# Kernel tuning notes

Hardware: AMD Instinct MI355X
Metric: run time of the kernel (lower is better)

The kernel has to match this reference:

```python
import jax, jax.numpy as jnp
import numpy as np

NUM_TOKENS = 2048
NUM_HEADS = 32
NUM_KV_HEADS = 8
HEAD_DIM = 128
ATTN_SCALE = 0.08838834764831845  # 1/sqrt(head_dim)


def setup_inputs() -> dict:
    key = jax.random.key(0)
    kq, kk, kv = jax.random.split(key, 3)
    q = jax.random.normal(kq, (NUM_TOKENS, NUM_HEADS, HEAD_DIM), dtype=jnp.float32)
    k = jax.random.normal(kk, (NUM_TOKENS, NUM_KV_HEADS, HEAD_DIM), dtype=jnp.float32)
    v = jax.random.normal(kv, (NUM_TOKENS, NUM_KV_HEADS, HEAD_DIM), dtype=jnp.float32)
    return {"q": q, "k": k, "v": v}


def reference(q, k, v):
    # Prefill path: all tokens attend causally; GQA expands kv heads.
    n_rep = NUM_HEADS // NUM_KV_HEADS
    k = jnp.repeat(k, n_rep, axis=1)  # (T, H, D)
    v = jnp.repeat(v, n_rep, axis=1)  # (T, H, D)
    # scores: (H, Tq, Tk)
    scores = jnp.einsum("thd,shd->hts", q, k) * ATTN_SCALE
    T = q.shape[0]
    causal = jnp.tril(jnp.ones((T, T), dtype=bool))  # (Tq, Tk)
    scores = jnp.where(causal[None, :, :], scores, -jnp.inf)
    weights = jax.nn.softmax(scores, axis=-1)
    out = jnp.einsum("hts,shd->thd", weights, v)  # (T, H, D)
    return out
```

## Files before the change

kernel.cpp:

```cpp
#include <hip/hip_runtime.h>

#define NT 2048
#define NH 32
#define NKV 8
#define HD 128
#define BM 128
#define BN 64
#define NQT (NT / BM)
#define SCALE_LOG2E 0.12754984003389239f
#define NEG_BIG -1.0e30f

typedef unsigned int   uint4v  __attribute__((ext_vector_type(4)));
typedef unsigned int   uint2v  __attribute__((ext_vector_type(2)));
typedef float          f32x4   __attribute__((ext_vector_type(4)));
typedef __bf16         bf16x8  __attribute__((ext_vector_type(8)));
typedef unsigned short u16;

#define PK 136
#define PV 72
#define PP 72
#define PO 136

__device__ __forceinline__ float bf2f(unsigned u) {
  return __builtin_bit_cast(float, u << 16);
}
__device__ __forceinline__ unsigned f2bf(float f) {
  unsigned u = __builtin_bit_cast(unsigned, f);
  u += 0x7fffu + ((u >> 16) & 1u);
  return u >> 16;
}

__global__ __launch_bounds__(256, 2)
void prep_kernel(const float* __restrict__ kg, const float* __restrict__ vg,
                 u16* __restrict__ wsk, u16* __restrict__ wsv) {
  __shared__ __align__(16) u16 lds_v[HD * PV];
  const int tid  = threadIdx.x;
  const int lane = tid & 63;
  const int w    = tid >> 6;
  const int hk   = blockIdx.x >> 5;
  const int jt   = blockIdx.x & 31;
  const int kv0  = jt * 64;

#pragma unroll
  for (int rr = 0; rr < 4; ++rr) {
    const int flat = rr * 256 + tid;
    const int row = flat >> 4, ch = flat & 15;
    const float* kp = &kg[((kv0 + row) * NKV + hk) * HD + ch * 8];
    const f32x4 a = *(const f32x4*)kp;
    const f32x4 b = *(const f32x4*)(kp + 4);
    uint4v pk;
    pk[0] = f2bf(a[0]) | (f2bf(a[1]) << 16);
    pk[1] = f2bf(a[2]) | (f2bf(a[3]) << 16);
    pk[2] = f2bf(b[0]) | (f2bf(b[1]) << 16);
    pk[3] = f2bf(b[2]) | (f2bf(b[3]) << 16);
    *(uint4v*)&wsk[(hk * NT + kv0 + row) * HD + ch * 8] = pk;
  }
#pragma unroll
  for (int rr = 0; rr < 4; ++rr) {
    const int d0 = (rr * 4 + w) * 8;
    const float* vp = &vg[((kv0 + lane) * NKV + hk) * HD + d0];
    const f32x4 a = *(const f32x4*)vp;
    const f32x4 b = *(const f32x4*)(vp + 4);
#pragma unroll
    for (int e = 0; e < 4; ++e) {
      lds_v[(d0 + e) * PV + lane]     = (u16)f2bf(a[e]);
      lds_v[(d0 + 4 + e) * PV + lane] = (u16)f2bf(b[e]);
    }
  }
  __syncthreads();
#pragma unroll
  for (int rr = 0; rr < 4; ++rr) {
    const int flat = rr * 256 + tid;
    const int row = flat >> 3, ch = flat & 7;
    *(uint4v*)&wsv[(hk * HD + row) * NT + kv0 + ch * 8] =
        *(uint4v*)&lds_v[row * PV + ch * 8];
  }
}

template <bool PRE>
__global__ __launch_bounds__(256, 2)
void fa_kernel(const float* __restrict__ qg, const float* __restrict__ kg,
               const float* __restrict__ vg, float* __restrict__ og,
               const u16* __restrict__ wsk, const u16* __restrict__ wsv) {
  __shared__ __align__(16) u16 lds_k[64 * PK];
  __shared__ __align__(16) u16 lds_v[HD * PV];
  __shared__ __align__(16) u16 lds_p[4 * 32 * PP];

  const int tid  = threadIdx.x;
  const int lane = tid & 63;
  const int w    = tid >> 6;
  const int quad = lane >> 4;
  const int l16  = lane & 15;

  const int h  = blockIdx.x;
  const int hk = h >> 2;
  const int y  = (int)blockIdx.y;
  const int qt = (y < NQT / 2) ? (NQT - 1 - y) : (y - NQT / 2);
  const int q0  = qt * BM;
  const int q0w = q0 + w * 32;

  uint4v qf[2][4];
#pragma unroll
  for (int qn = 0; qn < 2; ++qn)
#pragma unroll
    for (int c = 0; c < 4; ++c) {
      const int row = q0w + qn * 16 + l16;
      const float* qp = &qg[(row * NH + h) * HD + c * 32 + quad * 8];
      const f32x4 a = *(const f32x4*)qp;
      const f32x4 b = *(const f32x4*)(qp + 4);
      uint4v r;
      r[0] = f2bf(a[0] * SCALE_LOG2E) | (f2bf(a[1] * SCALE_LOG2E) << 16);
      r[1] = f2bf(a[2] * SCALE_LOG2E) | (f2bf(a[3] * SCALE_LOG2E) << 16);
      r[2] = f2bf(b[0] * SCALE_LOG2E) | (f2bf(b[1] * SCALE_LOG2E) << 16);
      r[3] = f2bf(b[2] * SCALE_LOG2E) | (f2bf(b[3] * SCALE_LOG2E) << 16);
      qf[qn][c] = r;
    }

  f32x4 o[8][2];
#pragma unroll
  for (int nt = 0; nt < 8; ++nt)
#pragma unroll
    for (int qn = 0; qn < 2; ++qn)
#pragma unroll
      for (int r = 0; r < 4; ++r) o[nt][qn][r] = 0.f;

  float l_run[2] = {0.f, 0.f};

  u16* pw = &lds_p[w * 32 * PP];

  const int njt = 2 * qt + 2;
  for (int jt = 0; jt < njt; ++jt) {
    const int kv0 = jt * BN;
    __syncthreads();

    if (PRE) {
#pragma unroll
      for (int rr = 0; rr < 4; ++rr) {
        const int flat = rr * 256 + tid;
        const int row = flat >> 4, ch = flat & 15;
        *(uint4v*)&lds_k[row * PK + ch * 8] =
            *(const uint4v*)&wsk[(hk * NT + kv0 + row) * HD + ch * 8];
      }
#pragma unroll
      for (int rr = 0; rr < 4; ++rr) {
        const int flat = rr * 256 + tid;
        const int row = flat >> 3, ch = flat & 7;
        *(uint4v*)&lds_v[row * PV + ch * 8] =
            *(const uint4v*)&wsv[(hk * HD + row) * NT + kv0 + ch * 8];
      }
    } else {
#pragma unroll
      for (int rr = 0; rr < 4; ++rr) {
        const int flat = rr * 256 + tid;
        const int row = flat >> 4, ch = flat & 15;
        const float* kp = &kg[((kv0 + row) * NKV + hk) * HD + ch * 8];
        const f32x4 a = *(const f32x4*)kp;
        const f32x4 b = *(const f32x4*)(kp + 4);
        uint4v pk;
        pk[0] = f2bf(a[0]) | (f2bf(a[1]) << 16);
        pk[1] = f2bf(a[2]) | (f2bf(a[3]) << 16);
        pk[2] = f2bf(b[0]) | (f2bf(b[1]) << 16);
        pk[3] = f2bf(b[2]) | (f2bf(b[3]) << 16);
        *(uint4v*)&lds_k[row * PK + ch * 8] = pk;
      }
#pragma unroll
      for (int rr = 0; rr < 4; ++rr) {
        const int d0 = (rr * 4 + w) * 8;
        const float* vp = &vg[((kv0 + lane) * NKV + hk) * HD + d0];
        const f32x4 a = *(const f32x4*)vp;
        const f32x4 b = *(const f32x4*)(vp + 4);
#pragma unroll
        for (int e = 0; e < 4; ++e) {
          lds_v[(d0 + e) * PV + lane]     = (u16)f2bf(a[e]);
          lds_v[(d0 + 4 + e) * PV + lane] = (u16)f2bf(b[e]);
        }
      }
    }
    __syncthreads();

    if (kv0 > q0w + 31) continue;

    f32x4 s[4][2];
#pragma unroll
    for (int mt = 0; mt < 4; ++mt)
#pragma unroll
      for (int qn = 0; qn < 2; ++qn)
#pragma unroll
        for (int r = 0; r < 4; ++r) s[mt][qn][r] = 0.f;

#pragma unroll
    for (int c = 0; c < 4; ++c) {
#pragma unroll
      for (int mt = 0; mt < 4; ++mt) {
        const uint4v kf = *(uint4v*)&lds_k[(mt * 16 + l16) * PK + c * 32 + quad * 8];
#pragma unroll
        for (int qn = 0; qn < 2; ++qn)
          s[mt][qn] = __builtin_amdgcn_mfma_f32_16x16x32_bf16(
              __builtin_bit_cast(bf16x8, kf),
              __builtin_bit_cast(bf16x8, qf[qn][c]), s[mt][qn], 0, 0, 0);
      }
    }

    if (kv0 + BN - 1 > q0w) {
#pragma unroll
      for (int mt = 0; mt < 4; ++mt)
#pragma unroll
        for (int qn = 0; qn < 2; ++qn)
#pragma unroll
          for (int r = 0; r < 4; ++r) {
            const int kvgl = kv0 + mt * 16 + quad * 4 + r;
            const int qgl  = q0w + qn * 16 + l16;
            if (kvgl > qgl) s[mt][qn][r] = NEG_BIG;
          }
    }

#pragma unroll
    for (int qn = 0; qn < 2; ++qn) {
      float ts = 0.f;
#pragma unroll
      for (int mt = 0; mt < 4; ++mt)
#pragma unroll
        for (int r = 0; r < 4; ++r) {
          const float p = exp2f(s[mt][qn][r]);
          s[mt][qn][r] = p;
          ts += p;
        }
      ts += __shfl_xor(ts, 16);
      ts += __shfl_xor(ts, 32);
      l_run[qn] += ts;

#pragma unroll
      for (int mt = 0; mt < 4; ++mt) {
        uint2v pk2;
        pk2[0] = f2bf(s[mt][qn][0]) | (f2bf(s[mt][qn][1]) << 16);
        pk2[1] = f2bf(s[mt][qn][2]) | (f2bf(s[mt][qn][3]) << 16);
        *(uint2v*)&pw[(qn * 16 + l16) * PP + mt * 16 + quad * 4] = pk2;
      }
    }

    __asm__ __volatile__("s_waitcnt lgkmcnt(0)" ::: "memory");

#pragma unroll
    for (int c2 = 0; c2 < 2; ++c2) {
      uint4v pf[2];
#pragma unroll
      for (int qn = 0; qn < 2; ++qn)
        pf[qn] = *(uint4v*)&pw[(qn * 16 + l16) * PP + c2 * 32 + quad * 8];
#pragma unroll
      for (int nt = 0; nt < 8; ++nt) {
        const uint4v vf = *(uint4v*)&lds_v[(nt * 16 + l16) * PV + c2 * 32 + quad * 8];
#pragma unroll
        for (int qn = 0; qn < 2; ++qn)
          o[nt][qn] = __builtin_amdgcn_mfma_f32_16x16x32_bf16(
              __builtin_bit_cast(bf16x8, vf),
              __builtin_bit_cast(bf16x8, pf[qn]), o[nt][qn], 0, 0, 0);
      }
    }
  }

  __syncthreads();

  u16* ob = (w < 2) ? &lds_k[w * 32 * PO] : &lds_v[(w - 2) * 32 * PO];

#pragma unroll
  for (int qn = 0; qn < 2; ++qn) {
    const float inv = 1.0f / l_run[qn];
#pragma unroll
    for (int nt = 0; nt < 8; ++nt) {
      uint2v ok2;
      ok2[0] = f2bf(o[nt][qn][0] * inv) | (f2bf(o[nt][qn][1] * inv) << 16);
      ok2[1] = f2bf(o[nt][qn][2] * inv) | (f2bf(o[nt][qn][3] * inv) << 16);
      *(uint2v*)&ob[(qn * 16 + l16) * PO + nt * 16 + quad * 4] = ok2;
    }
  }
  __asm__ __volatile__("s_waitcnt lgkmcnt(0)" ::: "memory");
#pragma unroll
  for (int rr = 0; rr < 8; ++rr) {
    const int idx = rr * 64 + lane;
    const int row = idx >> 4, ch = idx & 15;
    const uint4v ov = *(uint4v*)&ob[row * PO + ch * 8];
    f32x4 lo, hi;
    lo[0] = bf2f(ov[0] & 0xffffu); lo[1] = bf2f(ov[0] >> 16);
    lo[2] = bf2f(ov[1] & 0xffffu); lo[3] = bf2f(ov[1] >> 16);
    hi[0] = bf2f(ov[2] & 0xffffu); hi[1] = bf2f(ov[2] >> 16);
    hi[2] = bf2f(ov[3] & 0xffffu); hi[3] = bf2f(ov[3] >> 16);
    float* op = &og[((q0 + w * 32 + row) * NH + h) * HD + ch * 8];
    *(f32x4*)op       = lo;
    *(f32x4*)(op + 4) = hi;
  }
}

extern "C" void kernel_launch(void* const* d_in, const int* in_sizes, int n_in,
                              void* d_out, int out_size, void* d_ws, size_t ws_size,
                              hipStream_t stream) {
  (void)in_sizes; (void)n_in; (void)out_size;
  const float* q = (const float*)d_in[0];
  const float* k = (const float*)d_in[1];
  const float* v = (const float*)d_in[2];
  float* out = (float*)d_out;

  const size_t kv_bytes = (size_t)NKV * NT * HD * 2;
  dim3 grid(NH, NQT);
  if (ws_size >= 2 * kv_bytes) {
    u16* wsk = (u16*)d_ws;
    u16* wsv = wsk + (size_t)NKV * NT * HD;
    prep_kernel<<<dim3(NKV * 32), dim3(256), 0, stream>>>(k, v, wsk, wsv);
    fa_kernel<true><<<grid, dim3(256), 0, stream>>>(q, k, v, out, wsk, wsv);
  } else {
    fa_kernel<false><<<grid, dim3(256), 0, stream>>>(q, k, v, out, nullptr, nullptr);
  }
}
```

Baseline: 169.1 us.

## Double-buffer K/V tiles, pass P via shuffles, and cheapen bf16 packing

The attention kernel now double-buffers K and V tiles in LDS with register prefetch, so the global loads for the next tile overlap the MFMA work on the current one and the loop needs one barrier per tile instead of two. The P matrix is rearranged across lanes with shuffles instead of a round trip through LDS. The row-sum reduction is deferred to the end, exp2 uses the hardware builtin, and bf16 conversion uses round-half-up with a perm-based pack in place of round-to-nearest-even. The prep kernel is rewritten with smaller tiles and twice as many blocks. In exchange the kernel holds more LDS and registers, which may reduce occupancy, and rounding differs slightly from the old code.

New measurement: 149.8 us. -11.4%, faster.

```diff
diff --git a/kernel.cpp b/kernel.cpp
--- a/kernel.cpp
+++ b/kernel.cpp
@@ -18,62 +18,56 @@
 
 #define PK 136
 #define PV 72
-#define PP 72
 #define PO 136
 
 __device__ __forceinline__ float bf2f(unsigned u) {
   return __builtin_bit_cast(float, u << 16);
 }
 __device__ __forceinline__ unsigned f2bf(float f) {
-  unsigned u = __builtin_bit_cast(unsigned, f);
-  u += 0x7fffu + ((u >> 16) & 1u);
-  return u >> 16;
+  return (__builtin_bit_cast(unsigned, f) + 0x8000u) >> 16;
+}
+__device__ __forceinline__ unsigned pack_rn(float lo, float hi) {
+  const unsigned ul = __builtin_bit_cast(unsigned, lo) + 0x8000u;
+  const unsigned uh = __builtin_bit_cast(unsigned, hi) + 0x8000u;
+  return __builtin_amdgcn_perm(ul, uh, 0x03020706u);
 }
 
 __global__ __launch_bounds__(256, 2)
 void prep_kernel(const float* __restrict__ kg, const float* __restrict__ vg,
                  u16* __restrict__ wsk, u16* __restrict__ wsv) {
-  __shared__ __align__(16) u16 lds_v[HD * PV];
-  const int tid  = threadIdx.x;
-  const int lane = tid & 63;
-  const int w    = tid >> 6;
-  const int hk   = blockIdx.x >> 5;
-  const int jt   = blockIdx.x & 31;
-  const int kv0  = jt * 64;
-
-#pragma unroll
-  for (int rr = 0; rr < 4; ++rr) {
-    const int flat = rr * 256 + tid;
-    const int row = flat >> 4, ch = flat & 15;
-    const float* kp = &kg[((kv0 + row) * NKV + hk) * HD + ch * 8];
-    const f32x4 a = *(const f32x4*)kp;
-    const f32x4 b = *(const f32x4*)(kp + 4);
-    uint4v pk;
-    pk[0] = f2bf(a[0]) | (f2bf(a[1]) << 16);
-    pk[1] = f2bf(a[2]) | (f2bf(a[3]) << 16);
-    pk[2] = f2bf(b[0]) | (f2bf(b[1]) << 16);
-    pk[3] = f2bf(b[2]) | (f2bf(b[3]) << 16);
-    *(uint4v*)&wsk[(hk * NT + kv0 + row) * HD + ch * 8] = pk;
-  }
-#pragma unroll
-  for (int rr = 0; rr < 4; ++rr) {
-    const int d0 = (rr * 4 + w) * 8;
-    const float* vp = &vg[((kv0 + lane) * NKV + hk) * HD + d0];
-    const f32x4 a = *(const f32x4*)vp;
-    const f32x4 b = *(const f32x4*)(vp + 4);
-#pragma unroll
-    for (int e = 0; e < 4; ++e) {
-      lds_v[(d0 + e) * PV + lane]     = (u16)f2bf(a[e]);
-      lds_v[(d0 + 4 + e) * PV + lane] = (u16)f2bf(b[e]);
-    }
+  __shared__ __align__(16) float lds_f[32 * 132];
+  const int tid = threadIdx.x;
+  const int hk  = (int)blockIdx.x >> 6;
+  const int kv0 = ((int)blockIdx.x & 63) * 32;
+
+#pragma unroll
+  for (int r = 0; r < 4; ++r) {
+    const int flat = r * 256 + tid;
+    const int row = flat >> 5, q8 = flat & 31;
+    const f32x4 a = *(const f32x4*)&kg[((kv0 + row) * NKV + hk) * HD + q8 * 4];
+    uint2v pk;
+    pk[0] = pack_rn(a[0], a[1]);
+    pk[1] = pack_rn(a[2], a[3]);
+    *(uint2v*)&wsk[(hk * NT + kv0 + row) * HD + q8 * 4] = pk;
+  }
+#pragma unroll
+  for (int r = 0; r < 4; ++r) {
+    const int flat = r * 256 + tid;
+    const int row = flat >> 5, q8 = flat & 31;
+    *(f32x4*)&lds_f[row * 132 + q8 * 4] =
+        *(const f32x4*)&vg[((kv0 + row) * NKV + hk) * HD + q8 * 4];
   }
   __syncthreads();
-#pragma unroll
-  for (int rr = 0; rr < 4; ++rr) {
-    const int flat = rr * 256 + tid;
-    const int row = flat >> 3, ch = flat & 7;
-    *(uint4v*)&wsv[(hk * HD + row) * NT + kv0 + ch * 8] =
-        *(uint4v*)&lds_v[row * PV + ch * 8];
+  const int d = tid >> 1, half = tid & 1;
+#pragma unroll
+  for (int jj = 0; jj < 2; ++jj) {
+    const int j = half * 2 + jj;
+    uint4v outw;
+#pragma unroll
+    for (int e = 0; e < 4; ++e)
+      outw[e] = pack_rn(lds_f[(j * 8 + 2 * e) * 132 + d],
+                        lds_f[(j * 8 + 2 * e + 1) * 132 + d]);
+    *(uint4v*)&wsv[(hk * HD + d) * NT + kv0 + j * 8] = outw;
   }
 }
 
@@ -82,9 +76,8 @@
 void fa_kernel(const float* __restrict__ qg, const float* __restrict__ kg,
                const float* __restrict__ vg, float* __restrict__ og,
                const u16* __restrict__ wsk, const u16* __restrict__ wsv) {
-  __shared__ __align__(16) u16 lds_k[64 * PK];
-  __shared__ __align__(16) u16 lds_v[HD * PV];
-  __shared__ __align__(16) u16 lds_p[4 * 32 * PP];
+  __shared__ __align__(16) u16 lds_k[2][64 * PK];
+  __shared__ __align__(16) u16 lds_v[2][HD * PV];
 
   const int tid  = threadIdx.x;
   const int lane = tid & 63;
@@ -108,12 +101,12 @@
       const float* qp = &qg[(row * NH + h) * HD + c * 32 + quad * 8];
       const f32x4 a = *(const f32x4*)qp;
       const f32x4 b = *(const f32x4*)(qp + 4);
-      uint4v r;
-      r[0] = f2bf(a[0] * SCALE_LOG2E) | (f2bf(a[1] * SCALE_LOG2E) << 16);
-      r[1] = f2bf(a[2] * SCALE_LOG2E) | (f2bf(a[3] * SCALE_LOG2E) << 16);
-      r[2] = f2bf(b[0] * SCALE_LOG2E) | (f2bf(b[1] * SCALE_LOG2E) << 16);
-      r[3] = f2bf(b[2] * SCALE_LOG2E) | (f2bf(b[3] * SCALE_LOG2E) << 16);
-      qf[qn][c] = r;
+      uint4v rg;
+      rg[0] = pack_rn(a[0] * SCALE_LOG2E, a[1] * SCALE_LOG2E);
+      rg[1] = pack_rn(a[2] * SCALE_LOG2E, a[3] * SCALE_LOG2E);
+      rg[2] = pack_rn(b[0] * SCALE_LOG2E, b[1] * SCALE_LOG2E);
+      rg[3] = pack_rn(b[2] * SCALE_LOG2E, b[3] * SCALE_LOG2E);
+      qf[qn][c] = rg;
     }
 
   f32x4 o[8][2];
@@ -126,150 +119,189 @@
 
   float l_run[2] = {0.f, 0.f};
 
-  u16* pw = &lds_p[w * 32 * PP];
-
   const int njt = 2 * qt + 2;
+
+  uint4v kreg[4], vreg[4];
+  f32x4  kregf[4][2], vregf[4][2];
+
+  auto stage_load = [&](int jt) {
+    const int kvb = jt * BN;
+    if (PRE) {
+#pragma unroll
+      for (int r = 0; r < 4; ++r) {
+        const int flat = r * 256 + tid;
+        kreg[r] = *(const uint4v*)&wsk[(hk * NT + kvb + (flat >> 4)) * HD + (flat & 15) * 8];
+      }
+#pragma unroll
+      for (int r = 0; r < 4; ++r) {
+        const int flat = r * 256 + tid;
+        vreg[r] = *(const uint4v*)&wsv[(hk * HD + (flat >> 3)) * NT + kvb + (flat & 7) * 8];
+      }
+    } else {
+#pragma unroll
+      for (int r = 0; r < 4; ++r) {
+        const int flat = r * 256 + tid;
+        const float* kp = &kg[((kvb + (flat >> 4)) * NKV + hk) * HD + (flat & 15) * 8];
+        kregf[r][0] = *(const f32x4*)kp;
+        kregf[r][1] = *(const f32x4*)(kp + 4);
+      }
+#pragma unroll
+      for (int r = 0; r < 4; ++r) {
+        const int d0 = (r * 4 + w) * 8;
+        const float* vp = &vg[((kvb + lane) * NKV + hk) * HD + d0];
+        vregf[r][0] = *(const f32x4*)vp;
+        vregf[r][1] = *(const f32x4*)(vp + 4);
+      }
+    }
+  };
+  auto stage_write = [&](int b) {
+    if (PRE) {
+#pragma unroll
+      for (int r = 0; r < 4; ++r) {
+        const int flat = r * 256 + tid;
+        *(uint4v*)&lds_k[b][(flat >> 4) * PK + (flat & 15) * 8] = kreg[r];
+      }
+#pragma unroll
+      for (int r = 0; r < 4; ++r) {
+        const int flat = r * 256 + tid;
+        *(uint4v*)&lds_v[b][(flat >> 3) * PV + (flat & 7) * 8] = vreg[r];
+      }
+    } else {
+#pragma unroll
+      for (int r = 0; r < 4; ++r) {
+        const int flat = r * 256 + tid;
+        uint4v pk;
+        pk[0] = pack_rn(kregf[r][0][0], kregf[r][0][1]);
+        pk[1] = pack_rn(kregf[r][0][2], kregf[r][0][3]);
+        pk[2] = pack_rn(kregf[r][1][0], kregf[r][1][1]);
+        pk[3] = pack_rn(kregf[r][1][2], kregf[r][1][3]);
+        *(uint4v*)&lds_k[b][(flat >> 4) * PK + (flat & 15) * 8] = pk;
+      }
+#pragma unroll
+      for (int r = 0; r < 4; ++r) {
+        const int d0 = (r * 4 + w) * 8;
+#pragma unroll
+        for (int e = 0; e < 4; ++e) {
+          lds_v[b][(d0 + e) * PV + lane]     = (u16)f2bf(vregf[r][0][e]);
+          lds_v[b][(d0 + 4 + e) * PV + lane] = (u16)f2bf(vregf[r][1][e]);
+        }
+      }
+    }
+  };
+
+  const int sl0 = (quad & 1) * 32 + l16;
+  const int sl1 = sl0 + 16;
+  const bool qlo = (quad < 2);
+
+  stage_load(0);
+  stage_write(0);
+  __syncthreads();
+
   for (int jt = 0; jt < njt; ++jt) {
     const int kv0 = jt * BN;
-    __syncthreads();
-
-    if (PRE) {
-#pragma unroll
-      for (int rr = 0; rr < 4; ++rr) {
-        const int flat = rr * 256 + tid;
-        const int row = flat >> 4, ch = flat & 15;
-        *(uint4v*)&lds_k[row * PK + ch * 8] =
-            *(const uint4v*)&wsk[(hk * NT + kv0 + row) * HD + ch * 8];
-      }
-#pragma unroll
-      for (int rr = 0; rr < 4; ++rr) {
-        const int flat = rr * 256 + tid;
-        const int row = flat >> 3, ch = flat & 7;
-        *(uint4v*)&lds_v[row * PV + ch * 8] =
-            *(const uint4v*)&wsv[(hk * HD + row) * NT + kv0 + ch * 8];
-      }
-    } else {
-#pragma unroll
-      for (int rr = 0; rr < 4; ++rr) {
-        const int flat = rr * 256 + tid;
-        const int row = flat >> 4, ch = flat & 15;
-        const float* kp = &kg[((kv0 + row) * NKV + hk) * HD + ch * 8];
-        const f32x4 a = *(const f32x4*)kp;
-        const f32x4 b = *(const f32x4*)(kp + 4);
-        uint4v pk;
-        pk[0] = f2bf(a[0]) | (f2bf(a[1]) << 16);
-        pk[1] = f2bf(a[2]) | (f2bf(a[3]) << 16);
-        pk[2] = f2bf(b[0]) | (f2bf(b[1]) << 16);
-        pk[3] = f2bf(b[2]) | (f2bf(b[3]) << 16);
-        *(uint4v*)&lds_k[row * PK + ch * 8] = pk;
-      }
-#pragma unroll
-      for (int rr = 0; rr < 4; ++rr) {
-        const int d0 = (rr * 4 + w) * 8;
-        const float* vp = &vg[((kv0 + lane) * NKV + hk) * HD + d0];
-        const f32x4 a = *(const f32x4*)vp;
-        const f32x4 b = *(const f32x4*)(vp + 4);
-#pragma unroll
-        for (int e = 0; e < 4; ++e) {
-          lds_v[(d0 + e) * PV + lane]     = (u16)f2bf(a[e]);
-          lds_v[(d0 + 4 + e) * PV + lane] = (u16)f2bf(b[e]);
-        }
-      }
-    }
-    __syncthreads();
-
-    if (kv0 > q0w + 31) continue;
-
-    f32x4 s[4][2];
-#pragma unroll
-    for (int mt = 0; mt < 4; ++mt)
-#pragma unroll
-      for (int qn = 0; qn < 2; ++qn)
-#pragma unroll
-        for (int r = 0; r < 4; ++r) s[mt][qn][r] = 0.f;
-
-#pragma unroll
-    for (int c = 0; c < 4; ++c) {
-#pragma unroll
-      for (int mt = 0; mt < 4; ++mt) {
-        const uint4v kf = *(uint4v*)&lds_k[(mt * 16 + l16) * PK + c * 32 + quad * 8];
+    const int b   = jt & 1;
+    const bool havenext = (jt + 1 < njt);
+    if (havenext) stage_load(jt + 1);
+
+    if (kv0 <= q0w + 31) {
+      f32x4 s[4][2];
+#pragma unroll
+      for (int mt = 0; mt < 4; ++mt)
 #pragma unroll
         for (int qn = 0; qn < 2; ++qn)
-          s[mt][qn] = __builtin_amdgcn_mfma_f32_16x16x32_bf16(
-              __builtin_bit_cast(bf16x8, kf),
-              __builtin_bit_cast(bf16x8, qf[qn][c]), s[mt][qn], 0, 0, 0);
-      }
-    }
-
-    if (kv0 + BN - 1 > q0w) {
-#pragma unroll
-      for (int mt = 0; mt < 4; ++mt)
-#pragma unroll
-        for (int qn = 0; qn < 2; ++qn)
+#pragma unroll
+          for (int r = 0; r < 4; ++r) s[mt][qn][r] = 0.f;
+
+#pragma unroll
+      for (int c = 0; c < 4; ++c) {
+#pragma unroll
+        for (int mt = 0; mt < 4; ++mt) {
+          const uint4v kf = *(uint4v*)&lds_k[b][(mt * 16 + l16) * PK + c * 32 + quad * 8];
+#pragma unroll
+          for (int qn = 0; qn < 2; ++qn)
+            s[mt][qn] = __builtin_amdgcn_mfma_f32_16x16x32_bf16(
+                __builtin_bit_cast(bf16x8, kf),
+                __builtin_bit_cast(bf16x8, qf[qn][c]), s[mt][qn], 0, 0, 0);
+        }
+      }
+
+      if (kv0 + BN - 1 > q0w) {
+#pragma unroll
+        for (int mt = 0; mt < 4; ++mt)
+#pragma unroll
+          for (int qn = 0; qn < 2; ++qn)
+#pragma unroll
+            for (int r = 0; r < 4; ++r) {
+              const int kvgl = kv0 + mt * 16 + quad * 4 + r;
+              const int qgl  = q0w + qn * 16 + l16;
+              if (kvgl > qgl) s[mt][qn][r] = NEG_BIG;
+            }
+      }
+
+      unsigned pk[4][2][2];
+#pragma unroll
+      for (int qn = 0; qn < 2; ++qn) {
+        float ts = 0.f;
+#pragma unroll
+        for (int mt = 0; mt < 4; ++mt) {
 #pragma unroll
           for (int r = 0; r < 4; ++r) {
-            const int kvgl = kv0 + mt * 16 + quad * 4 + r;
-            const int qgl  = q0w + qn * 16 + l16;
-            if (kvgl > qgl) s[mt][qn][r] = NEG_BIG;
+            const float p = __builtin_amdgcn_exp2f(s[mt][qn][r]);
+            s[mt][qn][r] = p;
+            ts += p;
           }
-    }
-
-#pragma unroll
-    for (int qn = 0; qn < 2; ++qn) {
-      float ts = 0.f;
-#pragma unroll
-      for (int mt = 0; mt < 4; ++mt)
-#pragma unroll
-        for (int r = 0; r < 4; ++r) {
-          const float p = exp2f(s[mt][qn][r]);
-          s[mt][qn][r] = p;
-          ts += p;
-        }
-      ts += __shfl_xor(ts, 16);
-      ts += __shfl_xor(ts, 32);
-      l_run[qn] += ts;
-
-#pragma unroll
-      for (int mt = 0; mt < 4; ++mt) {
-        uint2v pk2;
-        pk2[0] = f2bf(s[mt][qn][0]) | (f2bf(s[mt][qn][1]) << 16);
-        pk2[1] = f2bf(s[mt][qn][2]) | (f2bf(s[mt][qn][3]) << 16);
-        *(uint2v*)&pw[(qn * 16 + l16) * PP + mt * 16 + quad * 4] = pk2;
-      }
-    }
-
-    __asm__ __volatile__("s_waitcnt lgkmcnt(0)" ::: "memory");
-
-#pragma unroll
-    for (int c2 = 0; c2 < 2; ++c2) {
-      uint4v pf[2];
-#pragma unroll
-      for (int qn = 0; qn < 2; ++qn)
-        pf[qn] = *(uint4v*)&pw[(qn * 16 + l16) * PP + c2 * 32 + quad * 8];
-#pragma unroll
-      for (int nt = 0; nt < 8; ++nt) {
-        const uint4v vf = *(uint4v*)&lds_v[(nt * 16 + l16) * PV + c2 * 32 + quad * 8];
-#pragma unroll
-        for (int qn = 0; qn < 2; ++qn)
-          o[nt][qn] = __builtin_amdgcn_mfma_f32_16x16x32_bf16(
-              __builtin_bit_cast(bf16x8, vf),
-              __builtin_bit_cast(bf16x8, pf[qn]), o[nt][qn], 0, 0, 0);
-      }
+          pk[mt][qn][0] = pack_rn(s[mt][qn][0], s[mt][qn][1]);
+          pk[mt][qn][1] = pack_rn(s[mt][qn][2], s[mt][qn][3]);
+        }
+        l_run[qn] += ts;
+      }
+
+#pragma unroll
+      for (int c2 = 0; c2 < 2; ++c2) {
+        uint4v pf[2];
+#pragma unroll
+        for (int p = 0; p < 4; ++p) {
+          const int sl = (p >> 1) ? sl1 : sl0;
+#pragma unroll
+          for (int qn = 0; qn < 2; ++qn) {
+            const int vA = __shfl((int)pk[2 * c2][qn][p & 1], sl);
+            const int vB = __shfl((int)pk[2 * c2 + 1][qn][p & 1], sl);
+            pf[qn][p] = (unsigned)(qlo ? vA : vB);
+          }
+        }
+#pragma unroll
+        for (int nt = 0; nt < 8; ++nt) {
+          const uint4v vf = *(uint4v*)&lds_v[b][(nt * 16 + l16) * PV + c2 * 32 + quad * 8];
+#pragma unroll
+          for (int qn = 0; qn < 2; ++qn)
+            o[nt][qn] = __builtin_amdgcn_mfma_f32_16x16x32_bf16(
+                __builtin_bit_cast(bf16x8, vf),
+                __builtin_bit_cast(bf16x8, pf[qn]), o[nt][qn], 0, 0, 0);
+        }
+      }
+    }
+
+    if (havenext) {
+      stage_write((jt + 1) & 1);
+      __syncthreads();
     }
   }
 
   __syncthreads();
 
-  u16* ob = (w < 2) ? &lds_k[w * 32 * PO] : &lds_v[(w - 2) * 32 * PO];
+  u16* ob = ((u16*)lds_k) + w * 32 * PO;
 
 #pragma unroll
   for (int qn = 0; qn < 2; ++qn) {
-    const float inv = 1.0f / l_run[qn];
+    float l = l_run[qn];
+    l += __shfl_xor(l, 16);
+    l += __shfl_xor(l, 32);
+    const float inv = 1.0f / l;
 #pragma unroll
     for (int nt = 0; nt < 8; ++nt) {
       uint2v ok2;
-      ok2[0] = f2bf(o[nt][qn][0] * inv) | (f2bf(o[nt][qn][1] * inv) << 16);
-      ok2[1] = f2bf(o[nt][qn][2] * inv) | (f2bf(o[nt][qn][3] * inv) << 16);
+      ok2[0] = pack_rn(o[nt][qn][0] * inv, o[nt][qn][1] * inv);
+      ok2[1] = pack_rn(o[nt][qn][2] * inv, o[nt][qn][3] * inv);
       *(uint2v*)&ob[(qn * 16 + l16) * PO + nt * 16 + quad * 4] = ok2;
     }
   }
@@ -304,7 +336,7 @@
   if (ws_size >= 2 * kv_bytes) {
     u16* wsk = (u16*)d_ws;
     u16* wsv = wsk + (size_t)NKV * NT * HD;
-    prep_kernel<<<dim3(NKV * 32), dim3(256), 0, stream>>>(k, v, wsk, wsv);
+    prep_kernel<<<dim3(NKV * 64), dim3(256), 0, stream>>>(k, v, wsk, wsv);
     fa_kernel<true><<<grid, dim3(256), 0, stream>>>(q, k, v, out, wsk, wsv);
   } else {
     fa_kernel<false><<<grid, dim3(256), 0, stream>>>(q, k, v, out, nullptr, nullptr);
```
